# Performance work log

Measured on AMD Instinct MI355X. Metric: run time of the kernel, lower is better.

Reference implementation:

```python
import jax, jax.numpy as jnp
import numpy as np

D = 64; H = 6; DH = 32; CB = 16; SB = 8; NSEL = 2; WIN = 7; OUT = 7; HID = 32
SCALE = DH ** -0.5
NEG = -3.4e38  # max_neg_value for fp32 masking


def _rope(x):
    # interleaved (lucidrains rotary-embedding-torch style), theta=10000
    n, d = x.shape[-2], x.shape[-1]
    inv = 1.0 / (10000.0 ** (jnp.arange(0, d, 2, dtype=jnp.float32) / d))
    fr = jnp.arange(n, dtype=jnp.float32)[:, None] * inv[None, :]  # n, d/2
    fr = jnp.repeat(fr, 2, axis=-1)                                # n, d
    c, s = jnp.cos(fr), jnp.sin(fr)
    xr = jnp.stack((-x[..., 1::2], x[..., 0::2]), axis=-1).reshape(x.shape)
    return x * c + xr * s


def reference(x, We, be, gamma, Wq, Wk, Wv, k_pos, v_pos, mem_k, mem_v,
              Wkc1, bkc1, Wkc2, bkc2, Wvc1, bvc1, Wvc2, bvc2,
              Wg, bg, Wo, Wh1, bh1, Wh2, bh2):
    B, N = x.shape
    nC = N // CB  # compressed blocks
    nF = N // SB  # fine/selection blocks

    # per-feature scalar embedding: Linear(1, 64)
    h = x[..., None] * We[0] + be  # B,N,D

    # RMSNorm (F.normalize * sqrt(D) * (gamma + 1))
    nrm = jnp.sqrt(jnp.sum(h * h, axis=-1, keepdims=True))
    hn = h / jnp.maximum(nrm, 1e-12) * jnp.sqrt(float(D)) * (gamma + 1.0)

    def proj(W):
        return jnp.einsum('bnd,de->bne', hn, W).reshape(B, N, H, DH).transpose(0, 2, 1, 3)
    q, k, v = proj(Wq), proj(Wk), proj(Wv)  # B,H,N,DH

    # ---- compressed branch (un-rotated q,k; intra-block pos emb + MLP compressor) ----
    kp = jnp.tile(k_pos, (1, nC, 1))  # H,N,DH
    vp = jnp.tile(v_pos, (1, nC, 1))
    CD = CB * DH
    kc_in = (k + kp).reshape(B, H, nC, CD)
    vc_in = (v + vp).reshape(B, H, nC, CD)
    ck = jax.nn.relu(kc_in @ Wkc1 + bkc1) @ Wkc2 + bkc2  # B,H,nC,DH
    cv = jax.nn.relu(vc_in @ Wvc1 + bvc1) @ Wvc2 + bvc2
    ck = jnp.concatenate([jnp.broadcast_to(mem_k, (B, H, 1, DH)), ck], axis=2)
    cv = jnp.concatenate([jnp.broadcast_to(mem_v, (B, H, 1, DH)), cv], axis=2)
    csim = jnp.einsum('bhid,bhjd->bhij', q, ck) * SCALE  # B,H,N,1+nC
    ck_last = jnp.concatenate([jnp.array([-1]), (jnp.arange(nC) + 1) * CB - 1])
    cmask = ck_last[None, :] < jnp.arange(N)[:, None]    # causal: block fully in past (mem kv always visible)
    csim = jnp.where(cmask, csim, NEG)
    c_out = jnp.einsum('bhij,bhjd->bhid', jax.nn.softmax(csim, axis=-1), cv)

    # ---- importance scores -> top-k selection blocks ----
    # compress_block_size != selection_block_size: repeat compressed scores, block-causal mask,
    # mean-pool to selection granularity (uniform within block -> direct mapping), pad+softmax
    rep = CB // SB
    imp = csim[..., 1:][..., jnp.arange(nF) // rep]  # B,H,N,nF
    qb = jnp.arange(N) // SB
    imp = jnp.where(qb[:, None] > jnp.arange(nF)[None, :], imp, NEG)  # strictly-past blocks only
    imp = jnp.concatenate([jnp.full(imp.shape[:-1] + (1,), -1e3, imp.dtype), imp], axis=-1)
    p = jax.nn.softmax(imp, axis=-1)[..., 1:]
    vals, idx = jax.lax.top_k(p, NSEL)  # B,H,N,NSEL

    # rotary only for fine + sliding branches
    qr, kr = _rope(q), _rope(k)

    # ---- fine (selected-block) branch ----
    sel = jnp.concatenate([idx, jnp.broadcast_to(qb[None, None, :, None], (B, H, N, 1))], axis=-1)  # own block appended
    kb = kr.reshape(B, H, nF, SB, DH)
    vb = v.reshape(B, H, nF, SB, DH)
    bi = jnp.arange(B)[:, None, None, None]
    hi = jnp.arange(H)[None, :, None, None]
    fk = kb[bi, hi, sel].reshape(B, H, N, (NSEL + 1) * SB, DH)
    fv = vb[bi, hi, sel].reshape(B, H, N, (NSEL + 1) * SB, DH)
    fmask_sel = jnp.repeat(vals > 1e-10, SB, axis=-1)                     # B,H,N,NSEL*SB
    own = jnp.arange(SB)[None, :] <= (jnp.arange(N) % SB)[:, None]        # causal within own block
    fmask = jnp.concatenate([fmask_sel, jnp.broadcast_to(own, (B, H, N, SB))], axis=-1)
    fsim = jnp.einsum('bhid,bhijd->bhij', qr, fk) * SCALE
    fsim = jnp.where(fmask, fsim, NEG)
    f_out = jnp.einsum('bhij,bhijd->bhid', jax.nn.softmax(fsim, axis=-1), fv)

    off = jnp.arange(WIN + 1)
    kidx = jnp.arange(N)[:, None] - off[None, :]
    valid = kidx >= 0
    kidx = jnp.maximum(kidx, 0)
    sk = kr[:, :, kidx]
    sv = v[:, :, kidx]
    ssim = jnp.einsum('bhid,bhiwd->bhiw', qr, sk) * SCALE
    ssim = jnp.where(valid, ssim, NEG)
    s_out = jnp.einsum('bhiw,bhiwd->bhid', jax.nn.softmax(ssim, axis=-1), sv)

    # ---- sigmoid-gated strategy combine (order: compressed, fine, sliding) ----
    g = jax.nn.sigmoid(jnp.einsum('bnd,de->bne', hn, Wg) + bg).reshape(B, N, H, 3).transpose(0, 2, 1, 3)
    out = g[..., 0:1] * c_out + g[..., 1:2] * f_out + g[..., 2:3] * s_out  # B,H,N,DH
    out = out.transpose(0, 2, 1, 3).reshape(B, N, H * DH) @ Wo             # B,N,D

    # model head: mean-pool over features, MLP
    pooled = out.mean(axis=1)
    hh = jax.nn.gelu(pooled @ Wh1 + bh1, approximate=False)
    return hh @ Wh2 + bh2


def setup_inputs() -> dict:
    key = jax.random.key(0)
    ks = jax.random.split(key, 20)
    B, N = 32, 512
    CD = CB * DH
    f32 = jnp.float32

    def rn(k, shape, fan_in):
        return jax.random.normal(k, shape, f32) / np.sqrt(fan_in)

    return {
        'x': jax.random.normal(ks[0], (B, N), f32),
        'We': rn(ks[1], (1, D), 1),
        'be': jnp.zeros((D,), f32),
        'gamma': 0.1 * jax.random.normal(ks[2], (D,), f32),
        'Wq': rn(ks[3], (D, H * DH), D),
        'Wk': rn(ks[4], (D, H * DH), D),
        'Wv': rn(ks[5], (D, H * DH), D),
        'k_pos': 0.02 * jax.random.normal(ks[6], (H, CB, DH), f32),
        'v_pos': 0.02 * jax.random.normal(ks[7], (H, CB, DH), f32),
        'mem_k': 0.02 * jax.random.normal(ks[8], (H, 1, DH), f32),
        'mem_v': 0.02 * jax.random.normal(ks[9], (H, 1, DH), f32),
        'Wkc1': rn(ks[10], (CD, CD), CD), 'bkc1': jnp.zeros((CD,), f32),
        'Wkc2': rn(ks[11], (CD, DH), CD), 'bkc2': jnp.zeros((DH,), f32),
        'Wvc1': rn(ks[12], (CD, CD), CD), 'bvc1': jnp.zeros((CD,), f32),
        'Wvc2': rn(ks[13], (CD, DH), CD), 'bvc2': jnp.zeros((DH,), f32),
        'Wg': rn(ks[14], (D, 3 * H), D),
        'bg': jnp.tile(jnp.array([-2.0, -2.0, 2.0], f32), H),
        'Wo': rn(ks[15], (H * DH, D), H * DH),
        'Wh1': rn(ks[16], (D, HID), D), 'bh1': jnp.zeros((HID,), f32),
        'Wh2': rn(ks[17], (HID, OUT), HID), 'bh2': jnp.zeros((OUT,), f32),
    }
```

## Files before the change

### kernel.cpp

```cpp
#include <hip/hip_runtime.h>

typedef unsigned short ushort_t;
typedef __attribute__((ext_vector_type(8))) short bf16x8;
typedef __attribute__((ext_vector_type(4))) float f32x4;

constexpr int N_   = 512;
constexpr int D_   = 64;
constexpr int H_   = 6;
constexpr int DH_  = 32;
constexpr int CB_  = 16;
constexpr int SB_  = 8;
constexpr int HD_  = H_ * DH_;
constexpr int CD_  = CB_ * DH_;
constexpr int nC_  = N_ / CB_;
constexpr int nF_  = N_ / SB_;
constexpr float SCALE_ = 0.17677669529663687f;
constexpr float NEG_ = -3.4e38f;

__device__ __forceinline__ ushort_t f2bf(float x) {
    unsigned u = __float_as_uint(x);
    unsigned r = u + 0x7FFFu + ((u >> 16) & 1u);
    return (ushort_t)(r >> 16);
}

__device__ __forceinline__ size_t frag_addr(int row, int k) {
    return (size_t)(row >> 4) * 8192 + (size_t)(k >> 5) * 512
         + (size_t)((k >> 3) & 3) * 128 + (size_t)(row & 15) * 8 + (k & 7);
}

__global__ __launch_bounds__(256) void k_cvtW(
    const float* __restrict__ Wk1, const float* __restrict__ Wv1,
    ushort_t* __restrict__ wtk_hi, ushort_t* __restrict__ wtk_lo,
    ushort_t* __restrict__ wtv_hi, ushort_t* __restrict__ wtv_lo)
{
    const float* W = blockIdx.z ? Wv1 : Wk1;
    ushort_t* ohi = blockIdx.z ? wtv_hi : wtk_hi;
    ushort_t* olo = blockIdx.z ? wtv_lo : wtk_lo;
    const int k0 = blockIdx.x * 64, j0 = blockIdx.y * 64;
    const int t = threadIdx.x;
    __shared__ float tile[64][65];
    #pragma unroll 4
    for (int i = 0; i < 16; ++i) {
        const int lin = t + i * 256;
        const int kk = lin >> 6, jj = lin & 63;
        tile[kk][jj] = W[(size_t)(k0 + kk) * 512 + j0 + jj];
    }
    __syncthreads();
    #pragma unroll 4
    for (int i = 0; i < 16; ++i) {
        const int lin = t + i * 256;
        const int jj = lin >> 6, kk = lin & 63;
        const float x = tile[kk][jj];
        const ushort_t h = f2bf(x);
        const float hf = __uint_as_float((unsigned)h << 16);
        const size_t fo = frag_addr(j0 + jj, k0 + kk);
        ohi[fo] = h;
        olo[fo] = f2bf(x - hf);
    }
}

__global__ __launch_bounds__(192) void k_embed(
    const float* __restrict__ x, const float* __restrict__ We, const float* __restrict__ be,
    const float* __restrict__ gamma,
    const float* __restrict__ Wq, const float* __restrict__ Wk, const float* __restrict__ Wv,
    const float* __restrict__ kpos, const float* __restrict__ vpos,
    const float* __restrict__ Wg, const float* __restrict__ bg,
    float* __restrict__ q, float* __restrict__ qr, float* __restrict__ kr,
    float* __restrict__ v,
    ushort_t* __restrict__ kin_hi, ushort_t* __restrict__ kin_lo,
    ushort_t* __restrict__ vin_hi, ushort_t* __restrict__ vin_lo,
    float* __restrict__ g)
{
    const int t  = threadIdx.x;
    const int wv = t >> 6;
    const int ln = t & 63;
    const int n00 = blockIdx.x * 16;
    const int b = n00 / N_;
    const int nbase = n00 % N_;

    __shared__ float hn[16][64];

    for (int r = wv; r < 16; r += 3) {
        const int n = nbase + r;
        float xv = x[b * N_ + n];
        float h = fmaf(xv, We[ln], be[ln]);
        float ss = h * h;
        #pragma unroll
        for (int off = 32; off; off >>= 1) ss += __shfl_down(ss, off);
        ss = __shfl(ss, 0);
        float sc = 8.0f / fmaxf(sqrtf(ss), 1e-12f);
        hn[r][ln] = h * sc * (gamma[ln] + 1.0f);
    }
    __syncthreads();

    const int e  = ln + (wv << 6);
    const int hh = e >> 5;
    const int dh = e & 31;
    float aq[16], ak[16], av[16];
    #pragma unroll
    for (int r = 0; r < 16; ++r) { aq[r] = 0.f; ak[r] = 0.f; av[r] = 0.f; }
    #pragma unroll 4
    for (int dd = 0; dd < 64; ++dd) {
        const float wq_ = Wq[dd * HD_ + e];
        const float wk_ = Wk[dd * HD_ + e];
        const float wv_ = Wv[dd * HD_ + e];
        #pragma unroll
        for (int r = 0; r < 16; ++r) {
            const float hv = hn[r][dd];
            aq[r] = fmaf(hv, wq_, aq[r]);
            ak[r] = fmaf(hv, wk_, ak[r]);
            av[r] = fmaf(hv, wv_, av[r]);
        }
    }
    const float invf = exp2f((float)(dh & ~1) * -0.41524101186092029f);
    #pragma unroll
    for (int r = 0; r < 16; ++r) {
        const int n = nbase + r;
        const size_t o = ((size_t)(b * H_ + hh) * N_ + n) * DH_ + dh;
        q[o] = aq[r];
        v[o] = av[r];
        const int pix = (hh * CB_ + (n & (CB_ - 1))) * DH_ + dh;
        const float kinv = ak[r] + kpos[pix];
        const float vinv = av[r] + vpos[pix];
        {
            const int row = (b * H_ + hh) * nC_ + (n >> 4);
            const int k   = (n & 15) * 32 + dh;
            const size_t fo = frag_addr(row, k);
            const ushort_t kh = f2bf(kinv);
            kin_hi[fo] = kh;
            kin_lo[fo] = f2bf(kinv - __uint_as_float((unsigned)kh << 16));
            const ushort_t vh = f2bf(vinv);
            vin_hi[fo] = vh;
            vin_lo[fo] = f2bf(vinv - __uint_as_float((unsigned)vh << 16));
        }
        const float aqp = __shfl_xor(aq[r], 1);
        const float akp = __shfl_xor(ak[r], 1);
        float sA, cA;
        __sincosf((float)n * invf, &sA, &cA);
        float rq, rk;
        if (dh & 1) { rq = fmaf(aqp, sA, aq[r] * cA); rk = fmaf(akp, sA, ak[r] * cA); }
        else        { rq = fmaf(-aqp, sA, aq[r] * cA); rk = fmaf(-akp, sA, ak[r] * cA); }
        qr[o] = rq; kr[o] = rk;
    }

    if (ln < 18) {
        for (int r = wv; r < 16; r += 3) {
            const int n = nbase + r;
            float a = bg[ln];
            for (int dd = 0; dd < 64; ++dd) a = fmaf(hn[r][dd], Wg[dd * 18 + ln], a);
            const float gv = 1.0f / (1.0f + __expf(-a));
            g[((size_t)(b * H_ + ln / 3) * N_ + n) * 3 + (ln % 3)] = gv;
        }
    }
}

__global__ __launch_bounds__(256) void k_compress(
    const ushort_t* __restrict__ kin_hi, const ushort_t* __restrict__ kin_lo,
    const ushort_t* __restrict__ vin_hi, const ushort_t* __restrict__ vin_lo,
    const ushort_t* __restrict__ wtk_hi, const ushort_t* __restrict__ wtk_lo,
    const ushort_t* __restrict__ wtv_hi, const ushort_t* __restrict__ wtv_lo,
    const float* __restrict__ bk1, const float* __restrict__ Wk2, const float* __restrict__ bk2,
    const float* __restrict__ bv1, const float* __restrict__ Wv2, const float* __restrict__ bv2,
    const float* __restrict__ mk, const float* __restrict__ mv,
    float* __restrict__ ck, float* __restrict__ cv)
{
    const bool isv = blockIdx.y != 0;
    const ushort_t* xhi = isv ? vin_hi : kin_hi;
    const ushort_t* xlo = isv ? vin_lo : kin_lo;
    const ushort_t* whi = isv ? wtv_hi : wtk_hi;
    const ushort_t* wlo = isv ? wtv_lo : wtk_lo;
    const float* b1 = isv ? bv1 : bk1;
    const float* W2 = isv ? Wv2 : Wk2;
    const float* b2 = isv ? bv2 : bk2;
    const float* mtok = isv ? mv : mk;
    float* outp = isv ? cv : ck;

    const int row0 = blockIdx.x * 32;
    const int t = threadIdx.x;
    const int w = t >> 6, l = t & 63;
    const int lrow = l & 15, kg = l >> 4;
    const int n0w = w * 128;

    __shared__ float hid[32 * 512];
    __shared__ float wred[4 * 16 * 32];

    if (t < 32) {
        outp[(size_t)blockIdx.x * 33 * DH_ + t] = mtok[(blockIdx.x % H_) * DH_ + t];
    }

    f32x4 acc[2][8];
    #pragma unroll
    for (int nt = 0; nt < 8; ++nt) {
        const float bv_ = b1[n0w + nt * 16 + lrow];
        #pragma unroll
        for (int mt = 0; mt < 2; ++mt) {
            acc[mt][nt][0] = bv_; acc[mt][nt][1] = bv_;
            acc[mt][nt][2] = bv_; acc[mt][nt][3] = bv_;
        }
    }
    const ushort_t* Ah = xhi + (size_t)(row0 >> 4) * 8192;
    const ushort_t* Al = xlo + (size_t)(row0 >> 4) * 8192;
    const ushort_t* Bh = whi + (size_t)(n0w >> 4) * 8192;
    const ushort_t* Bl = wlo + (size_t)(n0w >> 4) * 8192;
    const int lofs = l * 8;

    for (int ks = 0; ks < 16; ++ks) {
        const int kb = ks * 512 + lofs;
        const bf16x8 ah0 = *(const bf16x8*)(Ah + kb);
        const bf16x8 ah1 = *(const bf16x8*)(Ah + 8192 + kb);
        const bf16x8 al0 = *(const bf16x8*)(Al + kb);
        const bf16x8 al1 = *(const bf16x8*)(Al + 8192 + kb);
        #pragma unroll
        for (int nt = 0; nt < 8; ++nt) {
            const bf16x8 bh = *(const bf16x8*)(Bh + nt * 8192 + kb);
            const bf16x8 bl = *(const bf16x8*)(Bl + nt * 8192 + kb);
            acc[0][nt] = __builtin_amdgcn_mfma_f32_16x16x32_bf16(ah0, bh, acc[0][nt], 0, 0, 0);
            acc[0][nt] = __builtin_amdgcn_mfma_f32_16x16x32_bf16(ah0, bl, acc[0][nt], 0, 0, 0);
            acc[0][nt] = __builtin_amdgcn_mfma_f32_16x16x32_bf16(al0, bh, acc[0][nt], 0, 0, 0);
            acc[1][nt] = __builtin_amdgcn_mfma_f32_16x16x32_bf16(ah1, bh, acc[1][nt], 0, 0, 0);
            acc[1][nt] = __builtin_amdgcn_mfma_f32_16x16x32_bf16(ah1, bl, acc[1][nt], 0, 0, 0);
            acc[1][nt] = __builtin_amdgcn_mfma_f32_16x16x32_bf16(al1, bh, acc[1][nt], 0, 0, 0);
        }
    }
    #pragma unroll
    for (int mt = 0; mt < 2; ++mt) {
        #pragma unroll
        for (int nt = 0; nt < 8; ++nt) {
            const int col = n0w + nt * 16 + lrow;
            #pragma unroll
            for (int r = 0; r < 4; ++r) {
                const int row = mt * 16 + kg * 4 + r;
                hid[row * 512 + col] = fmaxf(acc[mt][nt][r], 0.0f);
            }
        }
    }
    __syncthreads();

    const int o = t & 31, seg = t >> 5;
    for (int half = 0; half < 2; ++half) {
        const int r0 = half * 16;
        float s[16];
        #pragma unroll
        for (int r = 0; r < 16; ++r) s[r] = 0.f;
        for (int di = 0; di < 64; ++di) {
            const int dd = seg * 64 + di;
            const float w2 = W2[(size_t)dd * 32 + o];
            #pragma unroll
            for (int r = 0; r < 16; ++r) s[r] = fmaf(hid[(r0 + r) * 512 + dd], w2, s[r]);
        }
        #pragma unroll
        for (int r = 0; r < 16; ++r) s[r] += __shfl_xor(s[r], 32);
        if (l < 32) {
            #pragma unroll
            for (int r = 0; r < 16; ++r) wred[(w * 16 + r) * 32 + o] = s[r];
        }
        __syncthreads();
        {
            const int rr = t >> 5;
            #pragma unroll
            for (int u = 0; u < 2; ++u) {
                const int r = rr + u * 8;
                const float val = wred[r * 32 + o] + wred[(16 + r) * 32 + o]
                                + wred[(32 + r) * 32 + o] + wred[(48 + r) * 32 + o] + b2[o];
                const int grow = row0 + r0 + r;
                outp[((size_t)(grow >> 5) * 33 + 1 + (grow & 31)) * DH_ + o] = val;
            }
        }
        __syncthreads();
    }
}

__global__ __launch_bounds__(256) void k_attn(
    const float* __restrict__ q, const float* __restrict__ qr,
    const float* __restrict__ kr, const float* __restrict__ v,
    const float* __restrict__ ck, const float* __restrict__ cv,
    const float* __restrict__ g, float* __restrict__ partial)
{
    const int t = threadIdx.x;
    const int sub = t & 3;
    const int wv = t >> 6;
    const int l = t & 63;
    const int bh = blockIdx.x >> 3;
    const int blk = blockIdx.x & 7;
    const int qi = t >> 2;
    const int n = blk * 64 + qi;
    const int qb = n >> 3;

    float qv[8];
    {
        const float4* p = (const float4*)(q + ((size_t)bh * N_ + n) * DH_ + sub * 8);
        const float4 f0 = p[0], f1 = p[1];
        qv[0]=f0.x; qv[1]=f0.y; qv[2]=f0.z; qv[3]=f0.w;
        qv[4]=f1.x; qv[5]=f1.y; qv[6]=f1.z; qv[7]=f1.w;
    }
    const float* ckb = ck + (size_t)bh * 33 * DH_;
    const float* cvb = cv + (size_t)bh * 33 * DH_;

    float mx = -INFINITY, den = 0.f;
    float cres[8];
    #pragma unroll
    for (int d = 0; d < 8; ++d) cres[d] = 0.f;
    float m2 = -1000.0f, sum2 = 1.0f;
    float v1 = -INFINITY, v2 = -INFINITY;
    int i1 = 0, i2 = 0;

    const int jend = 1 + max(n >> 4, (qb + 1) >> 1);
    for (int j = 0; j < jend; ++j) {
        float a = 0.f;
        {
            const float4* kp = (const float4*)(ckb + j * DH_ + sub * 8);
            const float4 f0 = kp[0], f1 = kp[1];
            a = fmaf(qv[0], f0.x, a); a = fmaf(qv[1], f0.y, a);
            a = fmaf(qv[2], f0.z, a); a = fmaf(qv[3], f0.w, a);
            a = fmaf(qv[4], f1.x, a); a = fmaf(qv[5], f1.y, a);
            a = fmaf(qv[6], f1.z, a); a = fmaf(qv[7], f1.w, a);
        }
        a += __shfl_xor(a, 1);
        a += __shfl_xor(a, 2);
        const bool ok = (j == 0) || (j * CB_ - 1 < n);
        a = ok ? a * SCALE_ : NEG_;

        float p;
        if (a > mx) {
            const float sc_ = __expf(mx - a);
            den *= sc_;
            #pragma unroll
            for (int d = 0; d < 8; ++d) cres[d] *= sc_;
            mx = a; p = 1.0f;
        } else {
            p = __expf(a - mx);
        }
        den += p;
        {
            const float4* vp = (const float4*)(cvb + j * DH_ + sub * 8);
            const float4 f0 = vp[0], f1 = vp[1];
            cres[0] = fmaf(p, f0.x, cres[0]); cres[1] = fmaf(p, f0.y, cres[1]);
            cres[2] = fmaf(p, f0.z, cres[2]); cres[3] = fmaf(p, f0.w, cres[3]);
            cres[4] = fmaf(p, f1.x, cres[4]); cres[5] = fmaf(p, f1.y, cres[5]);
            cres[6] = fmaf(p, f1.z, cres[6]); cres[7] = fmaf(p, f1.w, cres[7]);
        }

        if (j >= 1) {
            const int f0i = 2 * (j - 1);
            const int cnt = (qb > f0i) + (qb > f0i + 1);
            if (cnt) {
                if (a > m2) {
                    sum2 = fmaf(sum2, __expf(m2 - a), (float)cnt);
                    m2 = a;
                } else {
                    sum2 = fmaf((float)cnt, __expf(a - m2), sum2);
                }
                if (a > v1) {
                    if (cnt == 2) { v2 = a; i2 = f0i + 1; }
                    else          { v2 = v1; i2 = i1; }
                    v1 = a; i1 = f0i;
                } else if (a > v2) {
                    v2 = a; i2 = f0i;
                }
            }
        }
    }
    {
        const float invd = 1.0f / den;
        #pragma unroll
        for (int d = 0; d < 8; ++d) cres[d] *= invd;
    }
    const float isum = 1.0f / sum2;
    const bool bm0 = __expf(v1 - m2) * isum > 1e-10f;
    const bool bm1 = __expf(v2 - m2) * isum > 1e-10f;

    float qrv[8];
    {
        const float4* p = (const float4*)(qr + ((size_t)bh * N_ + n) * DH_ + sub * 8);
        const float4 f0 = p[0], f1 = p[1];
        qrv[0]=f0.x; qrv[1]=f0.y; qrv[2]=f0.z; qrv[3]=f0.w;
        qrv[4]=f1.x; qrv[5]=f1.y; qrv[6]=f1.z; qrv[7]=f1.w;
    }
    const float* krb = kr + (size_t)bh * N_ * DH_;
    const float* vb  = v  + (size_t)bh * N_ * DH_;

    int blocks[3]; bool bmask[3];
    blocks[0] = i1; blocks[1] = i2; blocks[2] = qb;
    bmask[0] = bm0; bmask[1] = bm1; bmask[2] = true;

    float fmx = -INFINITY, fden = 0.f;
    float fo[8];
    #pragma unroll
    for (int d = 0; d < 8; ++d) fo[d] = 0.f;
    #pragma unroll
    for (int s = 0; s < 3; ++s) {
        const int base = blocks[s] * SB_;
        #pragma unroll
        for (int j = 0; j < 8; ++j) {
            const int row = base + j;
            float a = 0.f;
            {
                const float4* kp = (const float4*)(krb + (size_t)row * DH_ + sub * 8);
                const float4 f0 = kp[0], f1 = kp[1];
                a = fmaf(qrv[0], f0.x, a); a = fmaf(qrv[1], f0.y, a);
                a = fmaf(qrv[2], f0.z, a); a = fmaf(qrv[3], f0.w, a);
                a = fmaf(qrv[4], f1.x, a); a = fmaf(qrv[5], f1.y, a);
                a = fmaf(qrv[6], f1.z, a); a = fmaf(qrv[7], f1.w, a);
            }
            a += __shfl_xor(a, 1);
            a += __shfl_xor(a, 2);
            const bool ok = (s < 2) ? bmask[s] : (j <= (n & 7));
            a = ok ? a * SCALE_ : NEG_;

            float p;
            if (a > fmx) {
                const float sc_ = __expf(fmx - a);
                fden *= sc_;
                #pragma unroll
                for (int d = 0; d < 8; ++d) fo[d] *= sc_;
                fmx = a; p = 1.0f;
            } else {
                p = __expf(a - fmx);
            }
            fden += p;
            const float4* vp = (const float4*)(vb + (size_t)row * DH_ + sub * 8);
            const float4 f0 = vp[0], f1 = vp[1];
            fo[0] = fmaf(p, f0.x, fo[0]); fo[1] = fmaf(p, f0.y, fo[1]);
            fo[2] = fmaf(p, f0.z, fo[2]); fo[3] = fmaf(p, f0.w, fo[3]);
            fo[4] = fmaf(p, f1.x, fo[4]); fo[5] = fmaf(p, f1.y, fo[5]);
            fo[6] = fmaf(p, f1.z, fo[6]); fo[7] = fmaf(p, f1.w, fo[7]);
        }
    }
    const float finv = 1.0f / fden;

    float wmx = -INFINITY, wden = 0.f;
    float so[8];
    #pragma unroll
    for (int d = 0; d < 8; ++d) so[d] = 0.f;
    #pragma unroll
    for (int w = 0; w < 8; ++w) {
        const int row = (n - w) >= 0 ? (n - w) : 0;
        float a;
        if (w <= n) {
            a = 0.f;
            const float4* kp = (const float4*)(krb + (size_t)row * DH_ + sub * 8);
            const float4 f0 = kp[0], f1 = kp[1];
            a = fmaf(qrv[0], f0.x, a); a = fmaf(qrv[1], f0.y, a);
            a = fmaf(qrv[2], f0.z, a); a = fmaf(qrv[3], f0.w, a);
            a = fmaf(qrv[4], f1.x, a); a = fmaf(qrv[5], f1.y, a);
            a = fmaf(qrv[6], f1.z, a); a = fmaf(qrv[7], f1.w, a);
            a += __shfl_xor(a, 1);
            a += __shfl_xor(a, 2);
            a *= SCALE_;
        } else a = NEG_;

        float p;
        if (a > wmx) {
            const float sc_ = __expf(wmx - a);
            wden *= sc_;
            #pragma unroll
            for (int d = 0; d < 8; ++d) so[d] *= sc_;
            wmx = a; p = 1.0f;
        } else {
            p = __expf(a - wmx);
        }
        wden += p;
        const float4* vp = (const float4*)(vb + (size_t)row * DH_ + sub * 8);
        const float4 f0 = vp[0], f1 = vp[1];
        so[0] = fmaf(p, f0.x, so[0]); so[1] = fmaf(p, f0.y, so[1]);
        so[2] = fmaf(p, f0.z, so[2]); so[3] = fmaf(p, f0.w, so[3]);
        so[4] = fmaf(p, f1.x, so[4]); so[5] = fmaf(p, f1.y, so[5]);
        so[6] = fmaf(p, f1.z, so[6]); so[7] = fmaf(p, f1.w, so[7]);
    }
    const float winv = 1.0f / wden;

    const float g0 = g[((size_t)bh * N_ + n) * 3];
    const float g1 = g[((size_t)bh * N_ + n) * 3 + 1];
    const float g2 = g[((size_t)bh * N_ + n) * 3 + 2];
    float o[8];
    #pragma unroll
    for (int d = 0; d < 8; ++d)
        o[d] = g0 * cres[d] + g1 * (fo[d] * finv) + g2 * (so[d] * winv);

    #pragma unroll
    for (int d = 0; d < 8; ++d) {
        o[d] += __shfl_down(o[d], 32);
        o[d] += __shfl_down(o[d], 16);
        o[d] += __shfl_down(o[d], 8);
        o[d] += __shfl_down(o[d], 4);
    }
    __shared__ float red[4][32];
    if (l < 4) {
        #pragma unroll
        for (int d = 0; d < 8; ++d) red[wv][l * 8 + d] = o[d];
    }
    __syncthreads();
    if (t < 32) {
        const float s = red[0][t] + red[1][t] + red[2][t] + red[3][t];
        partial[((size_t)bh * 8 + blk) * 32 + t] = s;
    }
}

__global__ void k_head(const float* __restrict__ partial, const float* __restrict__ Wo,
                       const float* __restrict__ Wh1, const float* __restrict__ bh1,
                       const float* __restrict__ Wh2, const float* __restrict__ bh2,
                       float* __restrict__ out)
{
    const int b = blockIdx.x;
    const int t = threadIdx.x;
    __shared__ float cs[192];
    __shared__ float pooled[64];
    __shared__ float hid[32];
    for (int i = t; i < 192; i += 64) {
        const int h = i >> 5, dh = i & 31;
        float s = 0.f;
        #pragma unroll
        for (int sg = 0; sg < 8; ++sg)
            s += partial[(((size_t)(b * H_ + h)) * 8 + sg) * 32 + dh];
        cs[i] = s;
    }
    __syncthreads();
    float a = 0.f;
    for (int e = 0; e < 192; ++e) a = fmaf(cs[e], Wo[e * 64 + t], a);
    pooled[t] = a * (1.0f / (float)N_);
    __syncthreads();
    if (t < 32) {
        float s = bh1[t];
        for (int d = 0; d < 64; ++d) s = fmaf(pooled[d], Wh1[d * 32 + t], s);
        hid[t] = 0.5f * s * (1.0f + erff(s * 0.7071067811865476f));
    }
    __syncthreads();
    if (t < 7) {
        float s = bh2[t];
        for (int j = 0; j < 32; ++j) s = fmaf(hid[j], Wh2[j * 7 + t], s);
        out[b * 7 + t] = s;
    }
}

extern "C" void kernel_launch(void* const* d_in, const int* in_sizes, int n_in,
                              void* d_out, int out_size, void* d_ws, size_t ws_size,
                              hipStream_t stream)
{
    const float* x     = (const float*)d_in[0];
    const float* We    = (const float*)d_in[1];
    const float* be    = (const float*)d_in[2];
    const float* gamma = (const float*)d_in[3];
    const float* Wq    = (const float*)d_in[4];
    const float* Wk    = (const float*)d_in[5];
    const float* Wv    = (const float*)d_in[6];
    const float* kpos  = (const float*)d_in[7];
    const float* vpos  = (const float*)d_in[8];
    const float* mk    = (const float*)d_in[9];
    const float* mv    = (const float*)d_in[10];
    const float* Wkc1  = (const float*)d_in[11];
    const float* bkc1  = (const float*)d_in[12];
    const float* Wkc2  = (const float*)d_in[13];
    const float* bkc2  = (const float*)d_in[14];
    const float* Wvc1  = (const float*)d_in[15];
    const float* bvc1  = (const float*)d_in[16];
    const float* Wvc2  = (const float*)d_in[17];
    const float* bvc2  = (const float*)d_in[18];
    const float* Wg    = (const float*)d_in[19];
    const float* bg    = (const float*)d_in[20];
    const float* Wo    = (const float*)d_in[21];
    const float* Wh1   = (const float*)d_in[22];
    const float* bh1   = (const float*)d_in[23];
    const float* Wh2   = (const float*)d_in[24];
    const float* bh2   = (const float*)d_in[25];
    float* out = (float*)d_out;

    const int B = in_sizes[0] / N_;
    const int BH = B * H_;
    const int BHN = BH * N_;
    const size_t SZ = (size_t)BHN * DH_;

    float* ws   = (float*)d_ws;
    float* q_   = ws;
    float* qr_  = ws + SZ;
    float* kr_  = ws + 2 * SZ;
    float* v_   = ws + 3 * SZ;
    ushort_t* kin_hi = (ushort_t*)(ws + 4 * SZ);
    ushort_t* kin_lo = kin_hi + SZ;
    ushort_t* vin_hi = kin_hi + 2 * SZ;
    ushort_t* vin_lo = kin_hi + 3 * SZ;
    float* ck_  = ws + 6 * SZ;
    float* cv_  = ck_ + (size_t)BH * 33 * DH_;
    float* g_   = cv_ + (size_t)BH * 33 * DH_;
    float* partial_ = g_ + (size_t)BHN * 3;
    ushort_t* wtk_hi = (ushort_t*)(partial_ + (size_t)BH * 8 * 32);
    ushort_t* wtk_lo = wtk_hi + 512 * 512;
    ushort_t* wtv_hi = wtk_hi + 2 * 512 * 512;
    ushort_t* wtv_lo = wtk_hi + 3 * 512 * 512;

    k_cvtW<<<dim3(8, 8, 2), dim3(256), 0, stream>>>(
        Wkc1, Wvc1, wtk_hi, wtk_lo, wtv_hi, wtv_lo);
    k_embed<<<dim3(B * N_ / 16), dim3(192), 0, stream>>>(
        x, We, be, gamma, Wq, Wk, Wv, kpos, vpos, Wg, bg,
        q_, qr_, kr_, v_, kin_hi, kin_lo, vin_hi, vin_lo, g_);
    k_compress<<<dim3(BH, 2), dim3(256), 0, stream>>>(
        kin_hi, kin_lo, vin_hi, vin_lo, wtk_hi, wtk_lo, wtv_hi, wtv_lo,
        bkc1, Wkc2, bkc2, bvc1, Wvc2, bvc2, mk, mv, ck_, cv_);
    k_attn<<<dim3(BHN / 64), dim3(256), 0, stream>>>(
        q_, qr_, kr_, v_, ck_, cv_, g_, partial_);
    k_head<<<dim3(B), dim3(64), 0, stream>>>(partial_, Wo, Wh1, bh1, Wh2, bh2, out);
}
```

Baseline: 148.0 us.

## Compute QKV projection with split-bf16 MFMA instead of scalar FMA

Adds a small kernel that converts Wq/Wk/Wv into hi/lo bf16 fragments laid out for MFMA. The embed kernel now packs normalized activations into bf16 hi/lo fragments in shared memory and does the 64x192 projections with 3-pass 16x16x32 bf16 MFMAs, which emulate fp32 accuracy. This replaces the per-thread scalar FMA loop and moves from 3 to 4 waves per block. It costs an extra kernel launch and a slight accuracy change from the split-bf16 approximation.

```diff
diff --git a/kernel.cpp b/kernel.cpp
--- a/kernel.cpp
+++ b/kernel.cpp
@@ -59,10 +59,31 @@
     }
 }
 
-__global__ __launch_bounds__(192) void k_embed(
+__global__ __launch_bounds__(256) void k_cvtP(
+    const float* __restrict__ Wq, const float* __restrict__ Wk,
+    const float* __restrict__ Wv,
+    ushort_t* __restrict__ pf_hi, ushort_t* __restrict__ pf_lo)
+{
+    const int m = blockIdx.x;
+    const float* W = m == 0 ? Wq : (m == 1 ? Wk : Wv);
+    ushort_t* ohi = pf_hi + m * 12288;
+    ushort_t* olo = pf_lo + m * 12288;
+    for (int i = threadIdx.x; i < 64 * 192; i += 256) {
+        const int dd = i / 192, e = i % 192;
+        const float xv = W[i];
+        const ushort_t h = f2bf(xv);
+        const float hf = __uint_as_float((unsigned)h << 16);
+        const int addr = (e >> 4) * 1024 + (dd >> 5) * 512
+                       + (((dd >> 3) & 3) * 16 + (e & 15)) * 8 + (dd & 7);
+        ohi[addr] = h;
+        olo[addr] = f2bf(xv - hf);
+    }
+}
+
+__global__ __launch_bounds__(256) void k_embed(
     const float* __restrict__ x, const float* __restrict__ We, const float* __restrict__ be,
     const float* __restrict__ gamma,
-    const float* __restrict__ Wq, const float* __restrict__ Wk, const float* __restrict__ Wv,
+    const ushort_t* __restrict__ pf_hi, const ushort_t* __restrict__ pf_lo,
     const float* __restrict__ kpos, const float* __restrict__ vpos,
     const float* __restrict__ Wg, const float* __restrict__ bg,
     float* __restrict__ q, float* __restrict__ qr, float* __restrict__ kr,
@@ -72,15 +93,16 @@
     float* __restrict__ g)
 {
     const int t  = threadIdx.x;
-    const int wv = t >> 6;
+    const int w  = t >> 6;
     const int ln = t & 63;
     const int n00 = blockIdx.x * 16;
     const int b = n00 / N_;
     const int nbase = n00 % N_;
 
-    __shared__ float hn[16][64];
-
-    for (int r = wv; r < 16; r += 3) {
+    __shared__ float hnf[16][64];
+    __shared__ ushort_t ahi[2][512], alo[2][512];
+
+    for (int r = w; r < 16; r += 4) {
         const int n = nbase + r;
         float xv = x[b * N_ + n];
         float h = fmaf(xv, We[ln], be[ln]);
@@ -89,65 +111,98 @@
         for (int off = 32; off; off >>= 1) ss += __shfl_down(ss, off);
         ss = __shfl(ss, 0);
         float sc = 8.0f / fmaxf(sqrtf(ss), 1e-12f);
-        hn[r][ln] = h * sc * (gamma[ln] + 1.0f);
+        const float val = h * sc * (gamma[ln] + 1.0f);
+        hnf[r][ln] = val;
+        const ushort_t hi = f2bf(val);
+        const int aidx = ((((ln & 31) >> 3) * 16 + r) << 3) + (ln & 7);
+        ahi[ln >> 5][aidx] = hi;
+        alo[ln >> 5][aidx] = f2bf(val - __uint_as_float((unsigned)hi << 16));
     }
     __syncthreads();
 
-    const int e  = ln + (wv << 6);
-    const int hh = e >> 5;
-    const int dh = e & 31;
-    float aq[16], ak[16], av[16];
-    #pragma unroll
-    for (int r = 0; r < 16; ++r) { aq[r] = 0.f; ak[r] = 0.f; av[r] = 0.f; }
-    #pragma unroll 4
-    for (int dd = 0; dd < 64; ++dd) {
-        const float wq_ = Wq[dd * HD_ + e];
-        const float wk_ = Wk[dd * HD_ + e];
-        const float wv_ = Wv[dd * HD_ + e];
-        #pragma unroll
-        for (int r = 0; r < 16; ++r) {
-            const float hv = hn[r][dd];
-            aq[r] = fmaf(hv, wq_, aq[r]);
-            ak[r] = fmaf(hv, wk_, ak[r]);
-            av[r] = fmaf(hv, wv_, av[r]);
-        }
-    }
-    const float invf = exp2f((float)(dh & ~1) * -0.41524101186092029f);
-    #pragma unroll
-    for (int r = 0; r < 16; ++r) {
-        const int n = nbase + r;
-        const size_t o = ((size_t)(b * H_ + hh) * N_ + n) * DH_ + dh;
-        q[o] = aq[r];
-        v[o] = av[r];
-        const int pix = (hh * CB_ + (n & (CB_ - 1))) * DH_ + dh;
-        const float kinv = ak[r] + kpos[pix];
-        const float vinv = av[r] + vpos[pix];
-        {
-            const int row = (b * H_ + hh) * nC_ + (n >> 4);
-            const int k   = (n & 15) * 32 + dh;
-            const size_t fo = frag_addr(row, k);
-            const ushort_t kh = f2bf(kinv);
-            kin_hi[fo] = kh;
-            kin_lo[fo] = f2bf(kinv - __uint_as_float((unsigned)kh << 16));
-            const ushort_t vh = f2bf(vinv);
-            vin_hi[fo] = vh;
-            vin_lo[fo] = f2bf(vinv - __uint_as_float((unsigned)vh << 16));
-        }
-        const float aqp = __shfl_xor(aq[r], 1);
-        const float akp = __shfl_xor(ak[r], 1);
-        float sA, cA;
-        __sincosf((float)n * invf, &sA, &cA);
-        float rq, rk;
-        if (dh & 1) { rq = fmaf(aqp, sA, aq[r] * cA); rk = fmaf(akp, sA, ak[r] * cA); }
-        else        { rq = fmaf(-aqp, sA, aq[r] * cA); rk = fmaf(-akp, sA, ak[r] * cA); }
-        qr[o] = rq; kr[o] = rk;
+    bf16x8 a_h[2], a_l[2];
+    a_h[0] = *(const bf16x8*)&ahi[0][ln * 8];
+    a_h[1] = *(const bf16x8*)&ahi[1][ln * 8];
+    a_l[0] = *(const bf16x8*)&alo[0][ln * 8];
+    a_l[1] = *(const bf16x8*)&alo[1][ln * 8];
+
+    f32x4 accQ[3], accK[3], accV[3];
+    #pragma unroll
+    for (int nt = 0; nt < 3; ++nt) {
+        #pragma unroll
+        for (int d = 0; d < 4; ++d) { accQ[nt][d] = 0.f; accK[nt][d] = 0.f; accV[nt][d] = 0.f; }
+    }
+
+    #pragma unroll
+    for (int nt = 0; nt < 3; ++nt) {
+        const int ct = w * 3 + nt;
+        #pragma unroll
+        for (int ks = 0; ks < 2; ++ks) {
+            const int off = ct * 1024 + ks * 512 + ln * 8;
+            const bf16x8 qh = *(const bf16x8*)(pf_hi + off);
+            const bf16x8 ql = *(const bf16x8*)(pf_lo + off);
+            const bf16x8 kh = *(const bf16x8*)(pf_hi + 12288 + off);
+            const bf16x8 kl = *(const bf16x8*)(pf_lo + 12288 + off);
+            const bf16x8 vh = *(const bf16x8*)(pf_hi + 24576 + off);
+            const bf16x8 vl = *(const bf16x8*)(pf_lo + 24576 + off);
+            accQ[nt] = __builtin_amdgcn_mfma_f32_16x16x32_bf16(a_h[ks], qh, accQ[nt], 0, 0, 0);
+            accQ[nt] = __builtin_amdgcn_mfma_f32_16x16x32_bf16(a_h[ks], ql, accQ[nt], 0, 0, 0);
+            accQ[nt] = __builtin_amdgcn_mfma_f32_16x16x32_bf16(a_l[ks], qh, accQ[nt], 0, 0, 0);
+            accK[nt] = __builtin_amdgcn_mfma_f32_16x16x32_bf16(a_h[ks], kh, accK[nt], 0, 0, 0);
+            accK[nt] = __builtin_amdgcn_mfma_f32_16x16x32_bf16(a_h[ks], kl, accK[nt], 0, 0, 0);
+            accK[nt] = __builtin_amdgcn_mfma_f32_16x16x32_bf16(a_l[ks], kh, accK[nt], 0, 0, 0);
+            accV[nt] = __builtin_amdgcn_mfma_f32_16x16x32_bf16(a_h[ks], vh, accV[nt], 0, 0, 0);
+            accV[nt] = __builtin_amdgcn_mfma_f32_16x16x32_bf16(a_h[ks], vl, accV[nt], 0, 0, 0);
+            accV[nt] = __builtin_amdgcn_mfma_f32_16x16x32_bf16(a_l[ks], vh, accV[nt], 0, 0, 0);
+        }
+    }
+
+    const int colr = ln & 15;
+    const int rowg = (ln >> 4) * 4;
+    #pragma unroll
+    for (int nt = 0; nt < 3; ++nt) {
+        const int e = w * 48 + nt * 16 + colr;
+        const int hh = e >> 5, dh = e & 31;
+        const float invf = exp2f((float)(dh & ~1) * -0.41524101186092029f);
+        #pragma unroll
+        for (int r = 0; r < 4; ++r) {
+            const int nl = rowg + r;
+            const int n = nbase + nl;
+            const size_t o = ((size_t)(b * H_ + hh) * N_ + n) * DH_ + dh;
+            const float aq = accQ[nt][r];
+            const float ak = accK[nt][r];
+            const float av = accV[nt][r];
+            q[o] = aq;
+            v[o] = av;
+            const int pix = (hh * CB_ + nl) * DH_ + dh;
+            const float kinv = ak + kpos[pix];
+            const float vinv = av + vpos[pix];
+            {
+                const int frow = (b * H_ + hh) * nC_ + (n >> 4);
+                const size_t fo = frag_addr(frow, nl * 32 + dh);
+                const ushort_t kh2 = f2bf(kinv);
+                kin_hi[fo] = kh2;
+                kin_lo[fo] = f2bf(kinv - __uint_as_float((unsigned)kh2 << 16));
+                const ushort_t vh2 = f2bf(vinv);
+                vin_hi[fo] = vh2;
+                vin_lo[fo] = f2bf(vinv - __uint_as_float((unsigned)vh2 << 16));
+            }
+            const float aqp = __shfl_xor(aq, 1);
+            const float akp = __shfl_xor(ak, 1);
+            float sA, cA;
+            __sincosf((float)n * invf, &sA, &cA);
+            float rq, rk;
+            if (dh & 1) { rq = fmaf(aqp, sA, aq * cA); rk = fmaf(akp, sA, ak * cA); }
+            else        { rq = fmaf(-aqp, sA, aq * cA); rk = fmaf(-akp, sA, ak * cA); }
+            qr[o] = rq; kr[o] = rk;
+        }
     }
 
     if (ln < 18) {
-        for (int r = wv; r < 16; r += 3) {
+        for (int r = w; r < 16; r += 4) {
             const int n = nbase + r;
             float a = bg[ln];
-            for (int dd = 0; dd < 64; ++dd) a = fmaf(hn[r][dd], Wg[dd * 18 + ln], a);
+            for (int dd = 0; dd < 64; ++dd) a = fmaf(hnf[r][dd], Wg[dd * 18 + ln], a);
             const float gv = 1.0f / (1.0f + __expf(-a));
             g[((size_t)(b * H_ + ln / 3) * N_ + n) * 3 + (ln % 3)] = gv;
         }
@@ -586,11 +641,15 @@
     ushort_t* wtk_lo = wtk_hi + 512 * 512;
     ushort_t* wtv_hi = wtk_hi + 2 * 512 * 512;
     ushort_t* wtv_lo = wtk_hi + 3 * 512 * 512;
+    ushort_t* pf_hi  = wtk_hi + 4 * 512 * 512;
+    ushort_t* pf_lo  = pf_hi + 3 * 12288;
 
     k_cvtW<<<dim3(8, 8, 2), dim3(256), 0, stream>>>(
         Wkc1, Wvc1, wtk_hi, wtk_lo, wtv_hi, wtv_lo);
-    k_embed<<<dim3(B * N_ / 16), dim3(192), 0, stream>>>(
-        x, We, be, gamma, Wq, Wk, Wv, kpos, vpos, Wg, bg,
+    k_cvtP<<<dim3(3), dim3(256), 0, stream>>>(
+        Wq, Wk, Wv, pf_hi, pf_lo);
+    k_embed<<<dim3(B * N_ / 16), dim3(256), 0, stream>>>(
+        x, We, be, gamma, pf_hi, pf_lo, kpos, vpos, Wg, bg,
         q_, qr_, kr_, v_, kin_hi, kin_lo, vin_hi, vin_lo, g_);
     k_compress<<<dim3(BH, 2), dim3(256), 0, stream>>>(
         kin_hi, kin_lo, vin_hi, vin_lo, wtk_hi, wtk_lo, wtv_hi, wtv_lo,
```

Result: slower. 153.3 us (+3.6%).
